# Performance work log

Hardware: AMD Instinct MI355X
Metric: run time of the kernel (lower is better)

Reference implementation:

```python
import math
import jax, jax.numpy as jnp
import numpy as np

EMBED_DIM = 1024
N_HEADS = 16
HEAD_DIM = EMBED_DIM // N_HEADS
B, T = 4, 2048


def setup_inputs() -> dict:
    key = jax.random.key(0)
    k1, k2, k3 = jax.random.split(key, 3)
    scale_in = 1.0 / math.sqrt(EMBED_DIM)
    return {
        "x": jax.random.normal(k1, (B, T, EMBED_DIM), dtype=jnp.float32),
        "direction": 0,  # 0=FORWARD (causal), 1=RETRODICTION (anti-causal), 2=CORRECTION (causal)
        "qkv_w": jax.random.normal(k2, (EMBED_DIM, 3 * EMBED_DIM), dtype=jnp.float32) * scale_in,
        "qkv_b": jnp.zeros((3 * EMBED_DIM,), dtype=jnp.float32),
        "proj_w": jax.random.normal(k3, (EMBED_DIM, EMBED_DIM), dtype=jnp.float32) * scale_in,
        "proj_b": jnp.zeros((EMBED_DIM,), dtype=jnp.float32),
    }


def reference(x, direction, qkv_w, qkv_b, proj_w, proj_b):
    Bx, Tx, C = x.shape
    qkv = x @ qkv_w + qkv_b                        # [B,T,3C]
    q, k, v = jnp.split(qkv, 3, axis=-1)
    # [B,T,C] -> [B,H,T,D]
    def heads(t):
        return t.reshape(Bx, Tx, N_HEADS, HEAD_DIM).transpose(0, 2, 1, 3)
    q, k, v = heads(q), heads(k), heads(v)
    scale = 1.0 / math.sqrt(HEAD_DIM)
    attn = jnp.einsum('bhqd,bhkd->bhqk', q, k) * scale
    rows = jnp.arange(Tx)[:, None]
    cols = jnp.arange(Tx)[None, :]
    if direction == 1:  # RETRODICTION -> anti-causal (upper triangular allowed)
        mask = cols >= rows
    else:               # FORWARD / CORRECTION -> causal
        mask = cols <= rows
    attn = jnp.where(mask[None, None], attn, -jnp.inf)
    attn = jax.nn.softmax(attn, axis=-1)  # dropout p=0 -> identity
    out = jnp.einsum('bhqk,bhkd->bhqd', attn, v)   # [B,H,T,D]
    out = out.transpose(0, 2, 1, 3).reshape(Bx, Tx, C)
    return out @ proj_w + proj_b
```

## Files before the change

kernel.cpp:

```cpp
#include <hip/hip_runtime.h>
#include <math.h>

typedef __bf16 bf16_t;
typedef bf16_t bf16x8 __attribute__((ext_vector_type(8)));
typedef bf16_t bf16x4 __attribute__((ext_vector_type(4)));
typedef float  f32x4  __attribute__((ext_vector_type(4)));
typedef float  floatv4 __attribute__((ext_vector_type(4)));

#define AS1 __attribute__((address_space(1)))
#define AS3 __attribute__((address_space(3)))

static __device__ __forceinline__ void gld_lds16(const void* g, void* l) {
  __builtin_amdgcn_global_load_lds((const AS1 unsigned int*)g,
                                   (AS3 unsigned int*)l, 16, 0, 0);
}
static __device__ __forceinline__ void block_sync() {
  asm volatile("" ::: "memory");
  __builtin_amdgcn_s_barrier();
  asm volatile("" ::: "memory");
}

__global__ __launch_bounds__(256) void k_cast(const float* __restrict__ in,
                                              bf16_t* __restrict__ out, int n4) {
  int i = blockIdx.x * 256 + threadIdx.x;
  if (i >= n4) return;
  floatv4 v = ((const floatv4*)in)[i];
  bf16x4 o;
  o.x = (bf16_t)v.x; o.y = (bf16_t)v.y; o.z = (bf16_t)v.z; o.w = (bf16_t)v.w;
  ((bf16x4*)out)[i] = o;
}

__global__ __launch_bounds__(256) void k_transpose_cast(const float* __restrict__ in,
                                                        bf16_t* __restrict__ out,
                                                        int R, int Cc) {
  __shared__ float tile[32][33];
  int c0 = blockIdx.x * 32, r0 = blockIdx.y * 32;
  int tx = threadIdx.x, ty = threadIdx.y;
#pragma unroll
  for (int i = 0; i < 32; i += 8)
    tile[ty + i][tx] = in[(size_t)(r0 + ty + i) * Cc + c0 + tx];
  __syncthreads();
#pragma unroll
  for (int i = 0; i < 32; i += 8)
    out[(size_t)(c0 + ty + i) * R + r0 + tx] = (bf16_t)tile[tx][ty + i];
}


__global__ __launch_bounds__(256, 3) void k_gemm_qkv(
    const bf16_t* __restrict__ A, const bf16_t* __restrict__ Bt,
    const float* __restrict__ bias,
    bf16_t* __restrict__ qo, bf16_t* __restrict__ ko, bf16_t* __restrict__ vto) {
  const int K = 1024;
  __shared__ __align__(16) char smem[49152];
  const int m0 = blockIdx.x * 128, n0 = blockIdx.y * 256;
  const int t = threadIdx.x, lane = t & 63, wv = t >> 6;
  const int ln15 = lane & 15, lhi = lane >> 4;

  f32x4 acc[8][4];
#pragma unroll
  for (int m = 0; m < 8; ++m)
#pragma unroll
    for (int n = 0; n < 4; ++n) acc[m][n] = (f32x4){0.f, 0.f, 0.f, 0.f};

  const bf16_t* aS = A + (size_t)(m0 + wv * 16 + ln15) * K + lhi * 8;
  const bf16_t* bS = Bt + (size_t)(n0 + wv * 16 + ln15) * K + lhi * 8;

  auto stage = [&](int k0, char* buf) {
    gld_lds16(aS + k0, buf + t * 16);
    gld_lds16(aS + (size_t)64 * K + k0, buf + 4096 + t * 16);
#pragma unroll
    for (int r = 0; r < 4; ++r)
      gld_lds16(bS + (size_t)r * 64 * K + k0, buf + 8192 + r * 4096 + t * 16);
  };

  stage(0, smem);
  asm volatile("s_waitcnt vmcnt(0)" ::: "memory");
  block_sync();

#pragma unroll 1
  for (int it = 0; it < 32; ++it) {
    char* bufC = smem + (it & 1) * 24576;
    char* bufN = smem + ((it + 1) & 1) * 24576;
    if (it + 1 < 32) stage((it + 1) * 32, bufN);
    const bf16_t* Ab = (const bf16_t*)bufC;
    const bf16_t* Bb = (const bf16_t*)(bufC + 8192);
    bf16x8 af[4], bfr[4];
#pragma unroll
    for (int n = 0; n < 4; ++n)
      bfr[n] = *(const bf16x8*)(Bb + (wv * 4 + n) * 512 + lane * 8);
#pragma unroll
    for (int h = 0; h < 2; ++h) {
#pragma unroll
      for (int m = 0; m < 4; ++m)
        af[m] = *(const bf16x8*)(Ab + (h * 4 + m) * 512 + lane * 8);
      asm volatile("s_waitcnt lgkmcnt(0)" ::: "memory");
      __builtin_amdgcn_sched_barrier(0);
      __builtin_amdgcn_s_setprio(1);
#pragma unroll
      for (int m = 0; m < 4; ++m)
#pragma unroll
        for (int n = 0; n < 4; ++n)
          acc[h * 4 + m][n] = __builtin_amdgcn_mfma_f32_16x16x32_bf16(af[m], bfr[n], acc[h * 4 + m][n], 0, 0, 0);
      __builtin_amdgcn_s_setprio(0);
    }
    asm volatile("s_waitcnt vmcnt(0)" ::: "memory");
    block_sync();
  }

  bf16_t* L = (bf16_t*)smem;
  const int bq = m0 >> 11, ttb = m0 & 2047;
  const int whichw = (n0 + (wv & 1) * 64 + (wv >> 1) * 128) >> 10;
  (void)whichw;
#pragma unroll 1
  for (int p = 0; p < 2; ++p) {
    const int whichp = (n0 + p * 128) >> 10;
    const float bscale = (whichp == 0) ? 0.18033688011112042f : 1.0f;
    if ((wv >> 1) == p) {
#pragma unroll
      for (int n = 0; n < 4; ++n) {
        const int colL = (wv & 1) * 64 + n * 16 + ln15;
        const float bv = bias[n0 + p * 128 + colL];
#pragma unroll
        for (int m = 0; m < 8; ++m)
#pragma unroll
          for (int j = 0; j < 4; ++j) {
            const int row = m * 16 + lhi * 4 + j;
            const bf16_t ob = (bf16_t)((acc[m][n][j] + bv) * bscale);
            if (whichp == 2) L[colL * 132 + row] = ob;
            else             L[row * 132 + colL] = ob;
          }
      }
    }
    block_sync();
    if (whichp == 2) {
#pragma unroll
      for (int c = 0; c < 8; ++c) {
        const int idx = c * 256 + t;
        const int vcol = idx >> 4, r8 = (idx & 15) * 8;
        bf16x8 v8 = *(const bf16x8*)&L[vcol * 132 + r8];
        const int cc = (n0 + p * 128 + vcol) & 1023;
        const int hh = cc >> 6, d = cc & 63;
        *(bf16x8*)&vto[((size_t)(bq * 16 + hh) * 64 + d) * 2048 + ttb + r8] = v8;
      }
    } else {
      bf16_t* dst = (whichp == 0) ? qo : ko;
#pragma unroll
      for (int c = 0; c < 8; ++c) {
        const int idx = c * 256 + t;
        const int row = idx >> 4, c8 = (idx & 15) * 8;
        bf16x8 v8 = *(const bf16x8*)&L[row * 132 + c8];
        const int cc = ((n0 & 1023) + p * 128) + c8;
        const int hh = cc >> 6, d = cc & 63;
        *(bf16x8*)&dst[((size_t)(bq * 16 + hh) * 2048 + ttb + row) * 64 + d] = v8;
      }
    }
    block_sync();
  }
}

__global__ __launch_bounds__(256) void k_attn3(
    const bf16_t* __restrict__ q, const bf16_t* __restrict__ k,
    const bf16_t* __restrict__ vt, const int* __restrict__ dirp,
    bf16_t* __restrict__ a2) {
  const int T = 2048;
  __shared__ __align__(16) bf16_t smem[16384];
  const int bh = blockIdx.x, b = bh >> 4, h = bh & 15;
  const int jb = blockIdx.y;
  const int t = threadIdx.x, lane = t & 63, w = t >> 6;
  const int ln15 = lane & 15, lhi = lane >> 4;
  const bool anti = (*dirp == 1);

  const bf16_t* kbase = k + (size_t)bh * T * 64;
  const bf16_t* vbase = vt + (size_t)bh * 64 * T;

  auto stage = [&](int kc0, int buf) {
    char* Kd = (char*)smem + buf * 16384;
    char* Vd = Kd + 8192;
#pragma unroll
    for (int s = 0; s < 2; ++s) {
      const int qk = s * 4 + (t >> 6);
      const int krow = kc0 + (qk >> 2) * 32 + ((qk >> 1) & 1) * 4 +
                       ((lane & 15) >> 2) * 8 + (lane & 3);
      const int kcolb = (lane >> 4) * 16 + (qk & 1) * 64;
      gld_lds16((const char*)kbase + (size_t)krow * 128 + kcolb,
                Kd + s * 4096 + t * 16);
      const int gv = qk;
      const int vd = (gv & 3) * 16 + (lane & 15);
      gld_lds16((const char*)vbase + (size_t)vd * 4096 + (size_t)kc0 * 2 +
                    (gv >> 2) * 64 + (lane >> 4) * 16,
                Vd + s * 4096 + t * 16);
    }
  };

#pragma unroll 1
  for (int sel = 0; sel < 2; ++sel) {
    const int qt = sel ? (31 - jb) : jb;
    const int q0 = qt * 64 + w * 16;
    const int qrow = q0 + ln15;

    const bf16_t* qp = q + ((size_t)bh * T + qrow) * 64 + lhi * 8;
    bf16x8 qf0 = *(const bf16x8*)qp;
    bf16x8 qf1 = *(const bf16x8*)(qp + 32);

    f32x4 acc[4];
#pragma unroll
    for (int g = 0; g < 4; ++g) acc[g] = (f32x4){0.f, 0.f, 0.f, 0.f};
    float mrun = -3.0e38f, lrun = 0.f;

    const int kt0 = anti ? qt : 0;
    const int nb = anti ? (32 - qt) : (qt + 1);

    stage(kt0 * 64, 0);
#pragma unroll 1
    for (int i = 0; i < nb; ++i) {
      const int kt = kt0 + i;
      const int buf = i & 1;
      if (i + 1 < nb) {
        stage((kt + 1) * 64, buf ^ 1);
        asm volatile("s_waitcnt vmcnt(4)" ::: "memory");
      } else {
        asm volatile("s_waitcnt vmcnt(0)" ::: "memory");
      }
      block_sync();
      const bf16_t* Kb = smem + buf * 8192;
      const bf16_t* Vb = Kb + 4096;

      float sc[16];
#pragma unroll
      for (int kh = 0; kh < 2; ++kh) {
        bf16x8 k0 = *(const bf16x8*)(Kb + (kh * 4 + 0) * 512 + lane * 8);
        bf16x8 k1 = *(const bf16x8*)(Kb + (kh * 4 + 1) * 512 + lane * 8);
        bf16x8 k2 = *(const bf16x8*)(Kb + (kh * 4 + 2) * 512 + lane * 8);
        bf16x8 k3 = *(const bf16x8*)(Kb + (kh * 4 + 3) * 512 + lane * 8);
        const f32x4 zz = (f32x4){0.f, 0.f, 0.f, 0.f};
        f32x4 slo = __builtin_amdgcn_mfma_f32_16x16x32_bf16(k0, qf0, zz, 0, 0, 0);
        slo = __builtin_amdgcn_mfma_f32_16x16x32_bf16(k1, qf1, slo, 0, 0, 0);
        f32x4 shi = __builtin_amdgcn_mfma_f32_16x16x32_bf16(k2, qf0, zz, 0, 0, 0);
        shi = __builtin_amdgcn_mfma_f32_16x16x32_bf16(k3, qf1, shi, 0, 0, 0);
#pragma unroll
        for (int j = 0; j < 4; ++j) {
          sc[kh * 8 + j] = slo[j];
          sc[kh * 8 + 4 + j] = shi[j];
        }
      }
      if (kt == qt) {
#pragma unroll
        for (int e = 0; e < 16; ++e) {
          const int col = kt * 64 + (e >> 3) * 32 + lhi * 8 + (e & 7);
          const bool ok = anti ? (col >= qrow) : (col <= qrow);
          sc[e] = ok ? sc[e] : -3.0e38f;
        }
      }
      float lmax = sc[0];
#pragma unroll
      for (int e = 1; e < 16; ++e) lmax = fmaxf(lmax, sc[e]);
      if (!__all(lmax <= mrun + 8.f)) {
        float vm = lmax;
        vm = fmaxf(vm, __shfl_xor(vm, 16));
        vm = fmaxf(vm, __shfl_xor(vm, 32));
        const float mn = fmaxf(mrun, vm);
        const float al = __builtin_amdgcn_exp2f(mrun - mn);
        lrun *= al;
#pragma unroll
        for (int g = 0; g < 4; ++g) acc[g] *= al;
        mrun = mn;
      }
      bf16x8 pb0, pb1;
      float rs = 0.f;
#pragma unroll
      for (int e = 0; e < 8; ++e) {
        float p = __builtin_amdgcn_exp2f(sc[e] - mrun);
        rs += p; pb0[e] = (bf16_t)p;
      }
#pragma unroll
      for (int e = 0; e < 8; ++e) {
        float p = __builtin_amdgcn_exp2f(sc[8 + e] - mrun);
        rs += p; pb1[e] = (bf16_t)p;
      }
      lrun += rs;
#pragma unroll
      for (int dg = 0; dg < 4; ++dg) {
        bf16x8 v0 = *(const bf16x8*)(Vb + dg * 512 + lane * 8);
        acc[dg] = __builtin_amdgcn_mfma_f32_16x16x32_bf16(v0, pb0, acc[dg], 0, 0, 0);
      }
#pragma unroll
      for (int dg = 0; dg < 4; ++dg) {
        bf16x8 v1 = *(const bf16x8*)(Vb + (4 + dg) * 512 + lane * 8);
        acc[dg] = __builtin_amdgcn_mfma_f32_16x16x32_bf16(v1, pb1, acc[dg], 0, 0, 0);
      }
      block_sync();
    }

    lrun += __shfl_xor(lrun, 16);
    lrun += __shfl_xor(lrun, 32);
    const float inv = __builtin_amdgcn_rcpf(lrun);
    bf16_t* op = a2 + ((size_t)b * T + qrow) * 1024 + h * 64 + lhi * 4;
#pragma unroll
    for (int g = 0; g < 4; ++g) {
      bf16x4 o4;
#pragma unroll
      for (int jx = 0; jx < 4; ++jx) o4[jx] = (bf16_t)(acc[g][jx] * inv);
      *(bf16x4*)(op + g * 16) = o4;
    }
  }
}

__global__ __launch_bounds__(256, 3) void k_gemm_proj(
    const bf16_t* __restrict__ A, const bf16_t* __restrict__ Bt,
    const float* __restrict__ bias, float* __restrict__ out) {
  const int K = 1024;
  __shared__ __align__(16) char smem[32768];
  const int m0 = blockIdx.x * 128, n0 = blockIdx.y * 128;
  const int t = threadIdx.x, lane = t & 63, wv = t >> 6;
  const int ln15 = lane & 15, lhi = lane >> 4;
  const int wr = wv >> 1, wcn = wv & 1;

  f32x4 acc[4][4];
#pragma unroll
  for (int m = 0; m < 4; ++m)
#pragma unroll
    for (int n = 0; n < 4; ++n) acc[m][n] = (f32x4){0.f, 0.f, 0.f, 0.f};

  const bf16_t* aS = A + (size_t)(m0 + wv * 16 + ln15) * K + lhi * 8;
  const bf16_t* bS = Bt + (size_t)(n0 + wv * 16 + ln15) * K + lhi * 8;

  auto stage = [&](int k0, char* buf) {
    gld_lds16(aS + k0, buf + t * 16);
    gld_lds16(aS + (size_t)64 * K + k0, buf + 4096 + t * 16);
    gld_lds16(bS + k0, buf + 8192 + t * 16);
    gld_lds16(bS + (size_t)64 * K + k0, buf + 12288 + t * 16);
  };

  stage(0, smem);
  asm volatile("s_waitcnt vmcnt(0)" ::: "memory");
  block_sync();

#pragma unroll 1
  for (int it = 0; it < 32; ++it) {
    char* bufC = smem + (it & 1) * 16384;
    char* bufN = smem + ((it + 1) & 1) * 16384;
    if (it + 1 < 32) stage((it + 1) * 32, bufN);
    const bf16_t* Ab = (const bf16_t*)bufC;
    const bf16_t* Bb = (const bf16_t*)(bufC + 8192);
    bf16x8 af[4], bfr[4];
#pragma unroll
    for (int m = 0; m < 4; ++m)
      af[m] = *(const bf16x8*)(Ab + (wr * 4 + m) * 512 + lane * 8);
#pragma unroll
    for (int n = 0; n < 4; ++n)
      bfr[n] = *(const bf16x8*)(Bb + (wcn * 4 + n) * 512 + lane * 8);
    asm volatile("s_waitcnt lgkmcnt(0)" ::: "memory");
    __builtin_amdgcn_sched_barrier(0);
    __builtin_amdgcn_s_setprio(1);
#pragma unroll
    for (int m = 0; m < 4; ++m)
#pragma unroll
      for (int n = 0; n < 4; ++n)
        acc[m][n] = __builtin_amdgcn_mfma_f32_16x16x32_bf16(af[m], bfr[n], acc[m][n], 0, 0, 0);
    __builtin_amdgcn_s_setprio(0);
    asm volatile("s_waitcnt vmcnt(0)" ::: "memory");
    block_sync();
  }

#pragma unroll
  for (int n = 0; n < 4; ++n) {
    const int col = n0 + wcn * 64 + n * 16 + ln15;
    const float bv = bias[col];
#pragma unroll
    for (int m = 0; m < 4; ++m)
#pragma unroll
      for (int j = 0; j < 4; ++j) {
        const int row = m0 + wr * 64 + m * 16 + lhi * 4 + j;
        out[(size_t)row * 1024 + col] = acc[m][n][j] + bv;
      }
  }
}

extern "C" void kernel_launch(void* const* d_in, const int* in_sizes, int n_in,
                              void* d_out, int out_size, void* d_ws, size_t ws_size,
                              hipStream_t stream) {
  (void)in_sizes; (void)n_in; (void)out_size; (void)ws_size;
  const float* x      = (const float*)d_in[0];
  const int*   dirp   = (const int*)d_in[1];
  const float* qkv_w  = (const float*)d_in[2];
  const float* qkv_b  = (const float*)d_in[3];
  const float* proj_w = (const float*)d_in[4];
  const float* proj_b = (const float*)d_in[5];
  float* out = (float*)d_out;

  char* ws = (char*)d_ws;
  bf16_t* xb   = (bf16_t*)(ws);
  bf16_t* wq_t = (bf16_t*)(ws + 16777216);
  bf16_t* wp_t = (bf16_t*)(ws + 23068672);
  bf16_t* qb   = (bf16_t*)(ws + 25165824);
  bf16_t* kb   = (bf16_t*)(ws + 41943040);
  bf16_t* vtb  = (bf16_t*)(ws + 58720256);
  bf16_t* a2   = xb;

  k_cast<<<8192, 256, 0, stream>>>(x, xb, 2097152);
  k_transpose_cast<<<dim3(96, 32), dim3(32, 8), 0, stream>>>(qkv_w, wq_t, 1024, 3072);
  k_transpose_cast<<<dim3(32, 32), dim3(32, 8), 0, stream>>>(proj_w, wp_t, 1024, 1024);
  k_gemm_qkv<<<dim3(64, 12), 256, 0, stream>>>(xb, wq_t, qkv_b, qb, kb, vtb);
  k_attn3<<<dim3(64, 16), 256, 0, stream>>>(qb, kb, vtb, dirp, a2);
  k_gemm_proj<<<dim3(64, 8), 256, 0, stream>>>(a2, wp_t, proj_b, out);
}
```

Baseline: 230.0 us.

## Enlarge GEMM tiles to 512 threads with triple-buffered interleaved LDS staging

Both projection GEMMs move to 512-thread blocks with larger tiles (256x384 for QKV, 256x128 for proj) arranged as a 2x4 wave grid. A three-buffer LDS ring prefetches two k-steps ahead, and the A and B loads are split across the two half-steps of MFMA work so global-to-LDS transfers overlap compute. The goal is more operand reuse per LDS byte and better latency hiding. In exchange, QKV now launches only 256 blocks on a large-CU device and uses about 120KB of LDS per block, which can limit occupancy and leave parts of the GPU idle.

```diff
diff --git a/kernel.cpp b/kernel.cpp
--- a/kernel.cpp
+++ b/kernel.cpp
@@ -45,111 +45,131 @@
     out[(size_t)(c0 + ty + i) * R + r0 + tx] = (bf16_t)tile[tx][ty + i];
 }
 
-
-__global__ __launch_bounds__(256, 3) void k_gemm_qkv(
+__global__ __launch_bounds__(512, 2) void k_gemm_qkv(
     const bf16_t* __restrict__ A, const bf16_t* __restrict__ Bt,
     const float* __restrict__ bias,
     bf16_t* __restrict__ qo, bf16_t* __restrict__ ko, bf16_t* __restrict__ vto) {
   const int K = 1024;
-  __shared__ __align__(16) char smem[49152];
-  const int m0 = blockIdx.x * 128, n0 = blockIdx.y * 256;
+  __shared__ __align__(16) char smem[122880];
+  const int m0 = blockIdx.x * 256, n0 = blockIdx.y * 384;
   const int t = threadIdx.x, lane = t & 63, wv = t >> 6;
   const int ln15 = lane & 15, lhi = lane >> 4;
-
-  f32x4 acc[8][4];
+  const int wr = wv >> 2, wc = wv & 3;
+
+  f32x4 acc[8][6];
 #pragma unroll
   for (int m = 0; m < 8; ++m)
 #pragma unroll
-    for (int n = 0; n < 4; ++n) acc[m][n] = (f32x4){0.f, 0.f, 0.f, 0.f};
+    for (int n = 0; n < 6; ++n) acc[m][n] = (f32x4){0.f, 0.f, 0.f, 0.f};
+  bf16x8 af[4], bfr[6];
 
   const bf16_t* aS = A + (size_t)(m0 + wv * 16 + ln15) * K + lhi * 8;
   const bf16_t* bS = Bt + (size_t)(n0 + wv * 16 + ln15) * K + lhi * 8;
-
-  auto stage = [&](int k0, char* buf) {
-    gld_lds16(aS + k0, buf + t * 16);
-    gld_lds16(aS + (size_t)64 * K + k0, buf + 4096 + t * 16);
-#pragma unroll
-    for (int r = 0; r < 4; ++r)
-      gld_lds16(bS + (size_t)r * 64 * K + k0, buf + 8192 + r * 4096 + t * 16);
+  const int dA = wv * 1024 + lane * 16;
+
+  auto stageA = [&](int k0, char* buf) {
+    gld_lds16(aS + k0, buf + dA);
+    gld_lds16(aS + (size_t)128 * K + k0, buf + 8192 + dA);
   };
-
-  stage(0, smem);
-  asm volatile("s_waitcnt vmcnt(0)" ::: "memory");
+  auto stageB = [&](int k0, char* buf) {
+    gld_lds16(bS + k0, buf + 16384 + dA);
+    gld_lds16(bS + (size_t)128 * K + k0, buf + 24576 + dA);
+    gld_lds16(bS + (size_t)256 * K + k0, buf + 32768 + dA);
+  };
+
+  char* b0 = smem;
+  char* b1 = smem + 40960;
+  char* b2 = smem + 81920;
+  stageA(0, b0); stageB(0, b0);
+  stageA(32, b1); stageB(32, b1);
+  asm volatile("s_waitcnt vmcnt(5)" ::: "memory");
   block_sync();
 
 #pragma unroll 1
   for (int it = 0; it < 32; ++it) {
-    char* bufC = smem + (it & 1) * 24576;
-    char* bufN = smem + ((it + 1) & 1) * 24576;
-    if (it + 1 < 32) stage((it + 1) * 32, bufN);
-    const bf16_t* Ab = (const bf16_t*)bufC;
-    const bf16_t* Bb = (const bf16_t*)(bufC + 8192);
-    bf16x8 af[4], bfr[4];
-#pragma unroll
-    for (int n = 0; n < 4; ++n)
-      bfr[n] = *(const bf16x8*)(Bb + (wv * 4 + n) * 512 + lane * 8);
-#pragma unroll
-    for (int h = 0; h < 2; ++h) {
-#pragma unroll
-      for (int m = 0; m < 4; ++m)
-        af[m] = *(const bf16x8*)(Ab + (h * 4 + m) * 512 + lane * 8);
-      asm volatile("s_waitcnt lgkmcnt(0)" ::: "memory");
-      __builtin_amdgcn_sched_barrier(0);
-      __builtin_amdgcn_s_setprio(1);
-#pragma unroll
-      for (int m = 0; m < 4; ++m)
-#pragma unroll
-        for (int n = 0; n < 4; ++n)
-          acc[h * 4 + m][n] = __builtin_amdgcn_mfma_f32_16x16x32_bf16(af[m], bfr[n], acc[h * 4 + m][n], 0, 0, 0);
-      __builtin_amdgcn_s_setprio(0);
-    }
-    asm volatile("s_waitcnt vmcnt(0)" ::: "memory");
-    block_sync();
+    const bool st = (it + 2 < 32);
+    const int k0n = (it + 2) * 32;
+#pragma unroll
+    for (int m = 0; m < 4; ++m)
+      af[m] = *(const bf16x8*)(b0 + (wr * 8 + m) * 1024 + lane * 16);
+#pragma unroll
+    for (int n = 0; n < 6; ++n)
+      bfr[n] = *(const bf16x8*)(b0 + 16384 + (wc * 6 + n) * 1024 + lane * 16);
+    if (st) stageA(k0n, b2);
+    block_sync();
+    asm volatile("s_waitcnt lgkmcnt(0)" ::: "memory");
+    __builtin_amdgcn_sched_barrier(0);
+    __builtin_amdgcn_s_setprio(1);
+#pragma unroll
+    for (int m = 0; m < 4; ++m)
+#pragma unroll
+      for (int n = 0; n < 6; ++n)
+        acc[m][n] = __builtin_amdgcn_mfma_f32_16x16x32_bf16(af[m], bfr[n], acc[m][n], 0, 0, 0);
+    __builtin_amdgcn_s_setprio(0);
+    block_sync();
+#pragma unroll
+    for (int m = 0; m < 4; ++m)
+      af[m] = *(const bf16x8*)(b0 + (wr * 8 + 4 + m) * 1024 + lane * 16);
+    if (st) stageB(k0n, b2);
+    block_sync();
+    asm volatile("s_waitcnt lgkmcnt(0)" ::: "memory");
+    __builtin_amdgcn_sched_barrier(0);
+    __builtin_amdgcn_s_setprio(1);
+#pragma unroll
+    for (int m = 0; m < 4; ++m)
+#pragma unroll
+      for (int n = 0; n < 6; ++n)
+        acc[4 + m][n] = __builtin_amdgcn_mfma_f32_16x16x32_bf16(af[m], bfr[n], acc[4 + m][n], 0, 0, 0);
+    __builtin_amdgcn_s_setprio(0);
+    if (st) asm volatile("s_waitcnt vmcnt(5)" ::: "memory");
+    else if (it + 1 < 32) asm volatile("s_waitcnt vmcnt(0)" ::: "memory");
+    block_sync();
+    char* tmp = b0; b0 = b1; b1 = b2; b2 = tmp;
   }
 
   bf16_t* L = (bf16_t*)smem;
   const int bq = m0 >> 11, ttb = m0 & 2047;
-  const int whichw = (n0 + (wv & 1) * 64 + (wv >> 1) * 128) >> 10;
-  (void)whichw;
 #pragma unroll 1
-  for (int p = 0; p < 2; ++p) {
-    const int whichp = (n0 + p * 128) >> 10;
-    const float bscale = (whichp == 0) ? 0.18033688011112042f : 1.0f;
-    if ((wv >> 1) == p) {
-#pragma unroll
-      for (int n = 0; n < 4; ++n) {
-        const int colL = (wv & 1) * 64 + n * 16 + ln15;
-        const float bv = bias[n0 + p * 128 + colL];
+  for (int p = 0; p < 3; ++p) {
+    const int wcol0 = n0 + p * 128;
+    const int which = wcol0 >> 10;
+    const float bscale = (which == 0) ? 0.18033688011112042f : 1.0f;
+#pragma unroll
+    for (int n = 0; n < 6; ++n) {
+      const int c16 = wc * 6 + n;
+      if ((c16 >> 3) == p) {
+        const int colL = c16 * 16 - p * 128 + ln15;
+        const float bv = bias[n0 + c16 * 16 + ln15];
 #pragma unroll
         for (int m = 0; m < 8; ++m)
 #pragma unroll
           for (int j = 0; j < 4; ++j) {
-            const int row = m * 16 + lhi * 4 + j;
+            const int row = wr * 128 + m * 16 + lhi * 4 + j;
             const bf16_t ob = (bf16_t)((acc[m][n][j] + bv) * bscale);
-            if (whichp == 2) L[colL * 132 + row] = ob;
-            else             L[row * 132 + colL] = ob;
+            if (which == 2) L[colL * 264 + row] = ob;
+            else            L[row * 132 + colL] = ob;
           }
       }
     }
     block_sync();
-    if (whichp == 2) {
+    if (which == 2) {
 #pragma unroll
       for (int c = 0; c < 8; ++c) {
-        const int idx = c * 256 + t;
-        const int vcol = idx >> 4, r8 = (idx & 15) * 8;
-        bf16x8 v8 = *(const bf16x8*)&L[vcol * 132 + r8];
-        const int cc = (n0 + p * 128 + vcol) & 1023;
+        const int idx = c * 512 + t;
+        const int vcol = idx >> 5, r8 = (idx & 31) * 8;
+        bf16x8 v8 = *(const bf16x8*)&L[vcol * 264 + r8];
+        const int cc = (wcol0 & 1023) + vcol;
         const int hh = cc >> 6, d = cc & 63;
         *(bf16x8*)&vto[((size_t)(bq * 16 + hh) * 64 + d) * 2048 + ttb + r8] = v8;
       }
     } else {
-      bf16_t* dst = (whichp == 0) ? qo : ko;
+      bf16_t* dst = (which == 0) ? qo : ko;
 #pragma unroll
       for (int c = 0; c < 8; ++c) {
-        const int idx = c * 256 + t;
+        const int idx = c * 512 + t;
         const int row = idx >> 4, c8 = (idx & 15) * 8;
         bf16x8 v8 = *(const bf16x8*)&L[row * 132 + c8];
-        const int cc = ((n0 & 1023) + p * 128) + c8;
+        const int cc = (wcol0 & 1023) + c8;
         const int hh = cc >> 6, d = cc & 63;
         *(bf16x8*)&dst[((size_t)(bq * 16 + hh) * 2048 + ttb + row) * 64 + d] = v8;
       }
@@ -305,72 +325,94 @@
   }
 }
 
-__global__ __launch_bounds__(256, 3) void k_gemm_proj(
+__global__ __launch_bounds__(512, 2) void k_gemm_proj(
     const bf16_t* __restrict__ A, const bf16_t* __restrict__ Bt,
     const float* __restrict__ bias, float* __restrict__ out) {
   const int K = 1024;
-  __shared__ __align__(16) char smem[32768];
-  const int m0 = blockIdx.x * 128, n0 = blockIdx.y * 128;
+  __shared__ __align__(16) char smem[73728];
+  const int m0 = blockIdx.x * 256, n0 = blockIdx.y * 128;
   const int t = threadIdx.x, lane = t & 63, wv = t >> 6;
   const int ln15 = lane & 15, lhi = lane >> 4;
-  const int wr = wv >> 1, wcn = wv & 1;
-
-  f32x4 acc[4][4];
-#pragma unroll
-  for (int m = 0; m < 4; ++m)
-#pragma unroll
-    for (int n = 0; n < 4; ++n) acc[m][n] = (f32x4){0.f, 0.f, 0.f, 0.f};
+  const int wr = wv >> 2, wc = wv & 3;
+
+  f32x4 acc[8][2];
+#pragma unroll
+  for (int m = 0; m < 8; ++m)
+#pragma unroll
+    for (int n = 0; n < 2; ++n) acc[m][n] = (f32x4){0.f, 0.f, 0.f, 0.f};
+  bf16x8 af[4], bfr[2];
 
   const bf16_t* aS = A + (size_t)(m0 + wv * 16 + ln15) * K + lhi * 8;
   const bf16_t* bS = Bt + (size_t)(n0 + wv * 16 + ln15) * K + lhi * 8;
-
-  auto stage = [&](int k0, char* buf) {
-    gld_lds16(aS + k0, buf + t * 16);
-    gld_lds16(aS + (size_t)64 * K + k0, buf + 4096 + t * 16);
-    gld_lds16(bS + k0, buf + 8192 + t * 16);
-    gld_lds16(bS + (size_t)64 * K + k0, buf + 12288 + t * 16);
+  const int dA = wv * 1024 + lane * 16;
+
+  auto stageA = [&](int k0, char* buf) {
+    gld_lds16(aS + k0, buf + dA);
+    gld_lds16(aS + (size_t)128 * K + k0, buf + 8192 + dA);
   };
-
-  stage(0, smem);
-  asm volatile("s_waitcnt vmcnt(0)" ::: "memory");
+  auto stageB = [&](int k0, char* buf) {
+    gld_lds16(bS + k0, buf + 16384 + dA);
+  };
+
+  char* b0 = smem;
+  char* b1 = smem + 24576;
+  char* b2 = smem + 49152;
+  stageA(0, b0); stageB(0, b0);
+  stageA(32, b1); stageB(32, b1);
+  asm volatile("s_waitcnt vmcnt(3)" ::: "memory");
   block_sync();
 
 #pragma unroll 1
   for (int it = 0; it < 32; ++it) {
-    char* bufC = smem + (it & 1) * 16384;
-    char* bufN = smem + ((it + 1) & 1) * 16384;
-    if (it + 1 < 32) stage((it + 1) * 32, bufN);
-    const bf16_t* Ab = (const bf16_t*)bufC;
-    const bf16_t* Bb = (const bf16_t*)(bufC + 8192);
-    bf16x8 af[4], bfr[4];
-#pragma unroll
-    for (int m = 0; m < 4; ++m)
-      af[m] = *(const bf16x8*)(Ab + (wr * 4 + m) * 512 + lane * 8);
-#pragma unroll
-    for (int n = 0; n < 4; ++n)
-      bfr[n] = *(const bf16x8*)(Bb + (wcn * 4 + n) * 512 + lane * 8);
+    const bool st = (it + 2 < 32);
+    const int k0n = (it + 2) * 32;
+#pragma unroll
+    for (int m = 0; m < 4; ++m)
+      af[m] = *(const bf16x8*)(b0 + (wr * 8 + m) * 1024 + lane * 16);
+#pragma unroll
+    for (int n = 0; n < 2; ++n)
+      bfr[n] = *(const bf16x8*)(b0 + 16384 + (wc * 2 + n) * 1024 + lane * 16);
+    if (st) stageA(k0n, b2);
+    block_sync();
     asm volatile("s_waitcnt lgkmcnt(0)" ::: "memory");
     __builtin_amdgcn_sched_barrier(0);
     __builtin_amdgcn_s_setprio(1);
 #pragma unroll
     for (int m = 0; m < 4; ++m)
 #pragma unroll
-      for (int n = 0; n < 4; ++n)
+      for (int n = 0; n < 2; ++n)
         acc[m][n] = __builtin_amdgcn_mfma_f32_16x16x32_bf16(af[m], bfr[n], acc[m][n], 0, 0, 0);
     __builtin_amdgcn_s_setprio(0);
-    asm volatile("s_waitcnt vmcnt(0)" ::: "memory");
-    block_sync();
+    block_sync();
+#pragma unroll
+    for (int m = 0; m < 4; ++m)
+      af[m] = *(const bf16x8*)(b0 + (wr * 8 + 4 + m) * 1024 + lane * 16);
+    if (st) stageB(k0n, b2);
+    block_sync();
+    asm volatile("s_waitcnt lgkmcnt(0)" ::: "memory");
+    __builtin_amdgcn_sched_barrier(0);
+    __builtin_amdgcn_s_setprio(1);
+#pragma unroll
+    for (int m = 0; m < 4; ++m)
+#pragma unroll
+      for (int n = 0; n < 2; ++n)
+        acc[4 + m][n] = __builtin_amdgcn_mfma_f32_16x16x32_bf16(af[m], bfr[n], acc[4 + m][n], 0, 0, 0);
+    __builtin_amdgcn_s_setprio(0);
+    if (st) asm volatile("s_waitcnt vmcnt(3)" ::: "memory");
+    else if (it + 1 < 32) asm volatile("s_waitcnt vmcnt(0)" ::: "memory");
+    block_sync();
+    char* tmp = b0; b0 = b1; b1 = b2; b2 = tmp;
   }
 
 #pragma unroll
-  for (int n = 0; n < 4; ++n) {
-    const int col = n0 + wcn * 64 + n * 16 + ln15;
+  for (int n = 0; n < 2; ++n) {
+    const int col = n0 + wc * 32 + n * 16 + ln15;
     const float bv = bias[col];
 #pragma unroll
-    for (int m = 0; m < 4; ++m)
+    for (int m = 0; m < 8; ++m)
 #pragma unroll
       for (int j = 0; j < 4; ++j) {
-        const int row = m0 + wr * 64 + m * 16 + lhi * 4 + j;
+        const int row = m0 + wr * 128 + m * 16 + lhi * 4 + j;
         out[(size_t)row * 1024 + col] = acc[m][n][j] + bv;
       }
   }
@@ -400,7 +442,7 @@
   k_cast<<<8192, 256, 0, stream>>>(x, xb, 2097152);
   k_transpose_cast<<<dim3(96, 32), dim3(32, 8), 0, stream>>>(qkv_w, wq_t, 1024, 3072);
   k_transpose_cast<<<dim3(32, 32), dim3(32, 8), 0, stream>>>(proj_w, wp_t, 1024, 1024);
-  k_gemm_qkv<<<dim3(64, 12), 256, 0, stream>>>(xb, wq_t, qkv_b, qb, kb, vtb);
+  k_gemm_qkv<<<dim3(32, 8), 512, 0, stream>>>(xb, wq_t, qkv_b, qb, kb, vtb);
   k_attn3<<<dim3(64, 16), 256, 0, stream>>>(qb, kb, vtb, dirp, a2);
-  k_gemm_proj<<<dim3(64, 8), 256, 0, stream>>>(a2, wp_t, proj_b, out);
-}
+  k_gemm_proj<<<dim3(32, 8), 512, 0, stream>>>(a2, wp_t, proj_b, out);
+}
```

New measurement: 197.5 us. -14.1%, faster.
